# Performance work log

Hardware: AMD Instinct MI355X
Metric: run time of the kernel (lower is better)

## Reference

```python
import jax, jax.numpy as jnp
import numpy as np

K = 9          # top-k neighbors
GROUPS = 4     # GroupNorm groups
EPS_GN = 1e-5  # torch GroupNorm default eps


def group_norm(x, gamma, beta):
    # x: [B, C, H, W]; normalize over (C/GROUPS, H, W) per group
    B, C, H, W = x.shape
    xg = x.reshape(B, GROUPS, -1)
    mu = xg.mean(axis=-1, keepdims=True)
    var = xg.var(axis=-1, keepdims=True)
    xn = ((xg - mu) / jnp.sqrt(var + EPS_GN)).reshape(B, C, H, W)
    return xn * gamma[None, :, None, None] + beta[None, :, None, None]


def setup_inputs() -> dict:
    key = jax.random.key(0)
    ks = jax.random.split(key, 6)
    B, C, H, W = 32, 128, 45, 45
    std = 1.0 / np.sqrt(C)
    x = jax.random.normal(ks[0], (B, C, H, W), dtype=jnp.float32)
    w1 = jax.random.uniform(ks[1], (C, C), jnp.float32, -std, std)
    b1 = jax.random.uniform(ks[2], (C,), jnp.float32, -std, std)
    w2 = jax.random.uniform(ks[3], (C, C), jnp.float32, -std, std)
    b2 = jax.random.uniform(ks[4], (C,), jnp.float32, -std, std)
    gamma1 = jnp.ones((C,), jnp.float32)
    beta1 = jnp.zeros((C,), jnp.float32)
    gamma2 = jnp.ones((C,), jnp.float32)
    beta2 = jnp.zeros((C,), jnp.float32)
    return {"x": x, "w1": w1, "b1": b1, "w2": w2, "b2": b2,
            "gamma1": gamma1, "beta1": beta1, "gamma2": gamma2, "beta2": beta2}


def reference(x, w1, b1, w2, b2, gamma1, beta1, gamma2, beta2):
    B, C, H, W = x.shape
    N = H * W
    # build_knn: flatten, L2-normalize, cosine sim, top-k
    xf = x.reshape(B, C, N).transpose(0, 2, 1)                  # [B, N, C]
    nrm = jnp.linalg.norm(xf, axis=-1, keepdims=True)
    xn = xf / jnp.maximum(nrm, 1e-12)                           # F.normalize
    sim = jnp.einsum('bnc,bmc->bnm', xn, xn)                    # [B, N, N]
    val, idx = jax.lax.top_k(sim, K)                            # [B, N, K]
    # normalized edge weights (shared by both GCN layers)
    v = val / (val.sum(axis=-1, keepdims=True) + 1e-6)          # [B, N, K]

    def gcn_apply(feat, w, b):
        xt = feat @ w                                           # [B, N, C]
        neigh = jax.vmap(lambda t, i: t[i])(xt, idx)            # [B, N, K, C]
        return jnp.einsum('bnkc,bnk->bnc', neigh, v) + b

    out = gcn_apply(xn, w1, b1)
    out = jax.nn.silu(group_norm(out.transpose(0, 2, 1).reshape(B, C, H, W), gamma1, beta1))
    of = out.reshape(B, C, N).transpose(0, 2, 1)
    out = gcn_apply(of, w2, b2)
    out = jax.nn.silu(group_norm(out.transpose(0, 2, 1).reshape(B, C, H, W), gamma2, beta2))
    return out
```

## Files before the change

kernel.cpp:

```cpp
#include <hip/hip_runtime.h>
#include <hip/hip_bf16.h>

#define BN 32
#define CC 128
#define NN 2025
#define KK 9
#define NGROUP 4
#define CPG 32
#define GN_EPS 1e-5f
#define ROWS_TOTAL (BN * NN)

typedef _Float16 f16;
typedef __attribute__((ext_vector_type(8))) _Float16 f16x8;
typedef __attribute__((ext_vector_type(4))) float f32x4;

#define S28 3.725290298461914e-09f
#define S40 9.094947017729282e-13f
#define RH  6.103515625e-05f
#define RL  1.4901161193847656e-08f

#define T0F 0.17f
#define CAP 128

__global__ __launch_bounds__(256) void k_normalize(const float* __restrict__ x,
                                                   f16* __restrict__ xh, f16* __restrict__ xl) {
    int wid  = blockIdx.x * 4 + (threadIdx.x >> 6);
    int lane = threadIdx.x & 63;
    int b = wid / NN;
    int n = wid - b * NN;
    float v0 = x[(b * CC + lane) * NN + n];
    float v1 = x[(b * CC + lane + 64) * NN + n];
    float ss = v0 * v0 + v1 * v1;
#pragma unroll
    for (int off = 32; off > 0; off >>= 1) ss += __shfl_xor(ss, off);
    float s = 1.0f / fmaxf(sqrtf(ss), 1e-12f);
    v0 *= s; v1 *= s;
    float w0 = v0 * 16384.0f, w1 = v1 * 16384.0f;
    f16 h0 = (f16)w0, h1 = (f16)w1;
    f16 l0 = (f16)((w0 - (float)h0) * 4096.0f);
    f16 l1 = (f16)((w1 - (float)h1) * 4096.0f);
    size_t base = (size_t)wid * CC;
    xh[base + lane] = h0;  xh[base + lane + 64] = h1;
    xl[base + lane] = l0;  xl[base + lane + 64] = l1;
}

__device__ __forceinline__ void ins9(float cand, int m, float* v, int* ix,
                                     float& mv, int& mi, int& mp) {
    bool take = (cand > mv) || ((cand == mv) && (m < mi));
    if (take) {
#pragma unroll
        for (int k = 0; k < 9; ++k) if (k == mp) { v[k] = cand; ix[k] = m; }
        float nv = v[0]; int ni = ix[0]; int np = 0;
#pragma unroll
        for (int k = 1; k < 9; ++k) {
            if (v[k] < nv || (v[k] == nv && ix[k] > ni)) { nv = v[k]; ni = ix[k]; np = k; }
        }
        mv = nv; mi = ni; mp = np;
    }
}

__global__ __launch_bounds__(256) void k_sim_topk(const f16* __restrict__ xh, const f16* __restrict__ xl,
                                                  float* __restrict__ vout, int* __restrict__ iout) {
    __shared__ float sv[32][CAP];
    __shared__ int   si[32][CAP];
    __shared__ int   cnt[32];
    __shared__ int   nbad;
    __shared__ int   badrows[32];

    const int b    = blockIdx.y;
    const int r0   = blockIdx.x * 32;
    const int t    = threadIdx.x;
    const int w    = t >> 6;
    const int lane = t & 63;
    const int jr   = lane & 15;
    const int q    = lane >> 4;

    if (t < 32) cnt[t] = 0;
    if (t == 0) nbad = 0;

    f16x8 bh[2][4], bl[2][4];
#pragma unroll
    for (int tile = 0; tile < 2; ++tile) {
        int rr = b * NN + min(r0 + tile * 16 + jr, NN - 1);
        const f16* pH = xh + (size_t)rr * CC;
        const f16* pL = xl + (size_t)rr * CC;
#pragma unroll
        for (int s = 0; s < 4; ++s) {
            bh[tile][s] = *(const f16x8*)(pH + s * 32 + q * 8);
            bl[tile][s] = *(const f16x8*)(pL + s * 32 + q * 8);
        }
    }
    __syncthreads();

    for (int chunk = 0; chunk < 32; ++chunk) {
        const int mb = chunk * 64 + w * 16;
        const int marow = b * NN + min(mb + jr, NN - 1);
        const f16* aHp = xh + (size_t)marow * CC;
        const f16* aLp = xl + (size_t)marow * CC;
        f32x4 h0 = {0.f, 0.f, 0.f, 0.f}, l0 = {0.f, 0.f, 0.f, 0.f};
        f32x4 h1 = {0.f, 0.f, 0.f, 0.f}, l1 = {0.f, 0.f, 0.f, 0.f};
#pragma unroll
        for (int s = 0; s < 4; ++s) {
            f16x8 ah = *(const f16x8*)(aHp + s * 32 + q * 8);
            f16x8 al = *(const f16x8*)(aLp + s * 32 + q * 8);
            h0 = __builtin_amdgcn_mfma_f32_16x16x32_f16(ah, bh[0][s], h0, 0, 0, 0);
            l0 = __builtin_amdgcn_mfma_f32_16x16x32_f16(ah, bl[0][s], l0, 0, 0, 0);
            l0 = __builtin_amdgcn_mfma_f32_16x16x32_f16(al, bh[0][s], l0, 0, 0, 0);
            h1 = __builtin_amdgcn_mfma_f32_16x16x32_f16(ah, bh[1][s], h1, 0, 0, 0);
            l1 = __builtin_amdgcn_mfma_f32_16x16x32_f16(ah, bl[1][s], l1, 0, 0, 0);
            l1 = __builtin_amdgcn_mfma_f32_16x16x32_f16(al, bh[1][s], l1, 0, 0, 0);
        }
#pragma unroll
        for (int reg = 0; reg < 4; ++reg) {
            int m = mb + q * 4 + reg;
            float c0 = h0[reg] * S28 + l0[reg] * S40;
            if (m < NN && c0 > T0F) {
                int pos = atomicAdd(&cnt[jr], 1);
                if (pos < CAP) { sv[jr][pos] = c0; si[jr][pos] = m; }
            }
            float c1 = h1[reg] * S28 + l1[reg] * S40;
            if (m < NN && c1 > T0F) {
                int pos = atomicAdd(&cnt[16 + jr], 1);
                if (pos < CAP) { sv[16 + jr][pos] = c1; si[16 + jr][pos] = m; }
            }
        }
    }
    __syncthreads();

    if (t < 32) {
        int r = r0 + t;
        if (r < NN) {
            int c = cnt[t];
            if (c >= 9 && c <= CAP) {
                float fv[9]; int fi[9];
#pragma unroll
                for (int k = 0; k < 9; ++k) { fv[k] = -3.0e38f; fi[k] = 0x7fffffff; }
                float mv = -3.0e38f; int mi = 0x7fffffff; int mp = 0;
                for (int j = 0; j < c; ++j) ins9(sv[t][j], si[t][j], fv, fi, mv, mi, mp);
                float s = 1e-6f;
#pragma unroll
                for (int k = 0; k < 9; ++k) s += fv[k];
                float inv = 1.0f / s;
                int base = (b * NN + r) * KK;
#pragma unroll
                for (int k = 0; k < 9; ++k) { vout[base + k] = fv[k] * inv; iout[base + k] = fi[k]; }
            } else {
                int slot = atomicAdd(&nbad, 1);
                badrows[slot] = r;
            }
        }
    }
    __syncthreads();

    if (w == 0) {
        int nb = nbad;
        for (int ib = 0; ib < nb; ++ib) {
            int r = badrows[ib];
            const f16* rH = xh + ((size_t)b * NN + r) * CC;
            const f16* rL = xl + ((size_t)b * NN + r) * CC;
            float fv[9]; int fi[9];
#pragma unroll
            for (int k = 0; k < 9; ++k) { fv[k] = -3.0e38f; fi[k] = 0x7fffffff; }
            float mv = -3.0e38f; int mi = 0x7fffffff; int mp = 0;
            for (int m = lane; m < NN; m += 64) {
                const f16* mH = xh + ((size_t)b * NN + m) * CC;
                const f16* mL = xl + ((size_t)b * NN + m) * CC;
                float a1 = 0.f, a2 = 0.f;
                for (int c2 = 0; c2 < CC; ++c2) {
                    float hr = (float)rH[c2], hm = (float)mH[c2];
                    float lr = (float)rL[c2], lm = (float)mL[c2];
                    a1 += hr * hm;
                    a2 += hr * lm + lr * hm;
                }
                ins9(a1 * S28 + a2 * S40, m, fv, fi, mv, mi, mp);
            }
#pragma unroll
            for (int off = 1; off < 64; off <<= 1) {
                float pv[9]; int pi[9];
#pragma unroll
                for (int k = 0; k < 9; ++k) { pv[k] = __shfl_xor(fv[k], off); pi[k] = __shfl_xor(fi[k], off); }
#pragma unroll
                for (int k = 0; k < 9; ++k) ins9(pv[k], pi[k], fv, fi, mv, mi, mp);
            }
            if (lane == 0) {
                float s = 1e-6f;
#pragma unroll
                for (int k = 0; k < 9; ++k) s += fv[k];
                float inv = 1.0f / s;
                int base = (b * NN + r) * KK;
#pragma unroll
                for (int k = 0; k < 9; ++k) { vout[base + k] = fv[k] * inv; iout[base + k] = fi[k]; }
            }
        }
    }
}

#define RST 36
__global__ __launch_bounds__(256) void k_gemm_hl(const f16* __restrict__ xh, const f16* __restrict__ xl,
                                                 const float* __restrict__ w, float* __restrict__ out) {
    __shared__ float rowsT[CC * RST];
    int t = threadIdx.x;
    int row0 = blockIdx.x * 32;
    for (int it = 0; it < 16; ++it) {
        int qq = t + it * 256;
        int c = qq & 127, r = qq >> 7;
        size_t idx = (size_t)(row0 + r) * CC + c;
        rowsT[c * RST + r] = (float)xh[idx] * RH + (float)xl[idx] * RL;
    }
    __syncthreads();
    int j = t & 127, half = t >> 7;
    float acc[16];
#pragma unroll
    for (int r = 0; r < 16; ++r) acc[r] = 0.0f;
    for (int c = 0; c < CC; ++c) {
        float wv = w[c * CC + j];
        const float4* ap = (const float4*)&rowsT[c * RST + half * 16];
        float4 a0 = ap[0], a1 = ap[1], a2 = ap[2], a3 = ap[3];
        acc[0]  += a0.x * wv; acc[1]  += a0.y * wv; acc[2]  += a0.z * wv; acc[3]  += a0.w * wv;
        acc[4]  += a1.x * wv; acc[5]  += a1.y * wv; acc[6]  += a1.z * wv; acc[7]  += a1.w * wv;
        acc[8]  += a2.x * wv; acc[9]  += a2.y * wv; acc[10] += a2.z * wv; acc[11] += a2.w * wv;
        acc[12] += a3.x * wv; acc[13] += a3.y * wv; acc[14] += a3.z * wv; acc[15] += a3.w * wv;
    }
#pragma unroll
    for (int r = 0; r < 16; ++r) out[(size_t)(row0 + half * 16 + r) * CC + j] = acc[r];
}

__global__ __launch_bounds__(256) void k_gemm(const float* __restrict__ in,
                                              const float* __restrict__ w,
                                              float* __restrict__ out) {
    __shared__ float rowsT[CC * RST];
    int t = threadIdx.x;
    int row0 = blockIdx.x * 32;
    for (int it = 0; it < 16; ++it) {
        int qq = t + it * 256;
        int c = qq & 127, r = qq >> 7;
        rowsT[c * RST + r] = in[(size_t)(row0 + r) * CC + c];
    }
    __syncthreads();
    int j = t & 127, half = t >> 7;
    float acc[16];
#pragma unroll
    for (int r = 0; r < 16; ++r) acc[r] = 0.0f;
    for (int c = 0; c < CC; ++c) {
        float wv = w[c * CC + j];
        const float4* ap = (const float4*)&rowsT[c * RST + half * 16];
        float4 a0 = ap[0], a1 = ap[1], a2 = ap[2], a3 = ap[3];
        acc[0]  += a0.x * wv; acc[1]  += a0.y * wv; acc[2]  += a0.z * wv; acc[3]  += a0.w * wv;
        acc[4]  += a1.x * wv; acc[5]  += a1.y * wv; acc[6]  += a1.z * wv; acc[7]  += a1.w * wv;
        acc[8]  += a2.x * wv; acc[9]  += a2.y * wv; acc[10] += a2.z * wv; acc[11] += a2.w * wv;
        acc[12] += a3.x * wv; acc[13] += a3.y * wv; acc[14] += a3.z * wv; acc[15] += a3.w * wv;
    }
#pragma unroll
    for (int r = 0; r < 16; ++r) out[(size_t)(row0 + half * 16 + r) * CC + j] = acc[r];
}

__global__ __launch_bounds__(256) void k_gather(const float* __restrict__ xt,
                                                const float* __restrict__ v,
                                                const int* __restrict__ idx,
                                                const float* __restrict__ bias,
                                                float* __restrict__ out) {
    int t = threadIdx.x;
    int g = blockIdx.x * 2 + (t >> 7);
    int c = t & 127;
    if (g >= ROWS_TOTAL) return;
    int b = g / NN;
    int nb = b * NN;
    float acc = bias[c];
    int base = g * KK;
#pragma unroll
    for (int k = 0; k < KK; ++k) {
        int   ii = idx[base + k];
        float vv = v[base + k];
        acc += vv * xt[(size_t)(nb + ii) * CC + c];
    }
    out[(size_t)g * CC + c] = acc;
}

__global__ __launch_bounds__(256) void k_gnstats(const float* __restrict__ xin,
                                                 float* __restrict__ stats) {
    int bg = blockIdx.x; int b = bg >> 2; int gg = bg & 3;
    size_t base = (size_t)b * (NN * CC) + gg * CPG;
    float s1 = 0.f, s2 = 0.f;
    for (int i = threadIdx.x; i < NN * CPG; i += 256) {
        float x = xin[base + (size_t)(i >> 5) * CC + (i & 31)];
        s1 += x; s2 += x * x;
    }
#pragma unroll
    for (int off = 32; off > 0; off >>= 1) { s1 += __shfl_xor(s1, off); s2 += __shfl_xor(s2, off); }
    __shared__ float r1[4], r2[4];
    int w = threadIdx.x >> 6;
    if ((threadIdx.x & 63) == 0) { r1[w] = s1; r2[w] = s2; }
    __syncthreads();
    if (threadIdx.x == 0) {
        float a = r1[0] + r1[1] + r1[2] + r1[3];
        float qq = r2[0] + r2[1] + r2[2] + r2[3];
        const float inv = 1.0f / (float)(NN * CPG);
        float mean = a * inv;
        float var = qq * inv - mean * mean;
        stats[bg * 2]     = mean;
        stats[bg * 2 + 1] = rsqrtf(fmaxf(var, 0.f) + GN_EPS);
    }
}

__global__ __launch_bounds__(256) void k_gnsilu(const float* __restrict__ xin,
                                                const float* __restrict__ stats,
                                                const float* __restrict__ gamma,
                                                const float* __restrict__ beta,
                                                float* __restrict__ out) {
    size_t e4 = ((size_t)blockIdx.x * 256 + threadIdx.x) * 4;
    int c0 = (int)(e4 & 127);
    int b  = (int)(e4 / (NN * CC));
    int gg = c0 >> 5;
    float mean = stats[(b * 4 + gg) * 2];
    float rstd = stats[(b * 4 + gg) * 2 + 1];
    float4 x = *(const float4*)&xin[e4];
    float g0 = gamma[c0], g1 = gamma[c0 + 1], g2 = gamma[c0 + 2], g3 = gamma[c0 + 3];
    float p0 = beta[c0],  p1 = beta[c0 + 1],  p2 = beta[c0 + 2],  p3 = beta[c0 + 3];
    float y0 = (x.x - mean) * rstd * g0 + p0;
    float y1 = (x.y - mean) * rstd * g1 + p1;
    float y2 = (x.z - mean) * rstd * g2 + p2;
    float y3 = (x.w - mean) * rstd * g3 + p3;
    float4 r;
    r.x = y0 / (1.0f + expf(-y0));
    r.y = y1 / (1.0f + expf(-y1));
    r.z = y2 / (1.0f + expf(-y2));
    r.w = y3 / (1.0f + expf(-y3));
    *(float4*)&out[e4] = r;
}

__global__ __launch_bounds__(256) void k_gnsilu_out(const float* __restrict__ xin,
                                                    const float* __restrict__ stats,
                                                    const float* __restrict__ gamma,
                                                    const float* __restrict__ beta,
                                                    float* __restrict__ out) {
    __shared__ float tile[32 * 65];
    int b = blockIdx.z, ct = blockIdx.y, nt = blockIdx.x;
    int c0 = ct * 32, n0 = nt * 64;
    int t = threadIdx.x;
    int cj = t & 31, ni0 = t >> 5;
    int gg = c0 >> 5;
    float mean = stats[(b * 4 + gg) * 2];
    float rstd = stats[(b * 4 + gg) * 2 + 1];
    float gm = gamma[c0 + cj];
    float bt = beta[c0 + cj];
#pragma unroll
    for (int i = 0; i < 8; ++i) {
        int n = n0 + ni0 + i * 8;
        if (n < NN) {
            float x = xin[((size_t)b * NN + n) * CC + c0 + cj];
            float y = (x - mean) * rstd * gm + bt;
            y = y / (1.0f + expf(-y));
            tile[cj * 65 + ni0 + i * 8] = y;
        }
    }
    __syncthreads();
    int nj = t & 63, ci0 = t >> 6;
#pragma unroll
    for (int i = 0; i < 8; ++i) {
        int c = ci0 + i * 4;
        int n = n0 + nj;
        if (n < NN) out[((size_t)b * CC + c0 + c) * NN + n] = tile[c * 65 + nj];
    }
}

extern "C" void kernel_launch(void* const* d_in, const int* in_sizes, int n_in,
                              void* d_out, int out_size, void* d_ws, size_t ws_size,
                              hipStream_t stream) {
    const float* x      = (const float*)d_in[0];
    const float* w1     = (const float*)d_in[1];
    const float* b1     = (const float*)d_in[2];
    const float* w2     = (const float*)d_in[3];
    const float* b2     = (const float*)d_in[4];
    const float* gamma1 = (const float*)d_in[5];
    const float* beta1  = (const float*)d_in[6];
    const float* gamma2 = (const float*)d_in[7];
    const float* beta2  = (const float*)d_in[8];
    float* out = (float*)d_out;

    const size_t BIG = (size_t)ROWS_TOTAL * CC;
    float* ws   = (float*)d_ws;
    float* bufB = ws;
    f16*   xh   = (f16*)(ws + BIG);
    f16*   xl   = xh + BIG;
    float* bufA = ws + BIG;
    float* vbuf = ws + 2 * BIG;
    int*   ibuf = (int*)(ws + 2 * BIG + (size_t)ROWS_TOTAL * KK);
    float* stats = ws + 2 * BIG + 2 * (size_t)ROWS_TOTAL * KK;

    k_normalize<<<ROWS_TOTAL / 4, 256, 0, stream>>>(x, xh, xl);
    k_sim_topk<<<dim3(64, BN), 256, 0, stream>>>(xh, xl, vbuf, ibuf);

    k_gemm_hl<<<(ROWS_TOTAL + 31) / 32, 256, 0, stream>>>(xh, xl, w1, bufB);
    k_gather<<<ROWS_TOTAL / 2, 256, 0, stream>>>(bufB, vbuf, ibuf, b1, bufA);
    k_gnstats<<<BN * NGROUP, 256, 0, stream>>>(bufA, stats);
    k_gnsilu<<<(int)(BIG / 1024), 256, 0, stream>>>(bufA, stats, gamma1, beta1, bufB);

    k_gemm<<<(ROWS_TOTAL + 31) / 32, 256, 0, stream>>>(bufB, w2, bufA);
    k_gather<<<ROWS_TOTAL / 2, 256, 0, stream>>>(bufA, vbuf, ibuf, b2, bufB);
    k_gnstats<<<BN * NGROUP, 256, 0, stream>>>(bufB, stats);
    k_gnsilu_out<<<dim3((NN + 63) / 64, NGROUP, BN), 256, 0, stream>>>(bufB, stats, gamma2, beta2, out);
}
```

Baseline: 760.3 us.

## Double-buffer A-tile loads in sim/top-k loop and shrink candidate LDS buffers

The similarity loop now prefetches the next 64-row chunk's hi/lo fp16 A fragments into a second register set while the current chunk runs its MFMAs and threshold filtering. This is meant to hide global-load latency behind compute. Candidate indices in shared memory are stored as unsigned short, and both candidate arrays get padded row strides, which cuts LDS footprint and bank conflicts during the per-row scan. The cost is more VGPRs for the second fragment buffer, which may reduce occupancy.

```diff
diff --git a/kernel.cpp b/kernel.cpp
--- a/kernel.cpp
+++ b/kernel.cpp
@@ -59,10 +59,50 @@
     }
 }
 
+
+#define LOADA(CH, AH, AL) do {                                              \
+    int mb_ = (CH) * 64 + w * 16;                                           \
+    size_t ar_ = (size_t)(b * NN + min(mb_ + jr, NN - 1)) * CC;             \
+    const f16* pH_ = xh + ar_;                                              \
+    const f16* pL_ = xl + ar_;                                              \
+    _Pragma("unroll")                                                       \
+    for (int s_ = 0; s_ < 4; ++s_) {                                        \
+        AH[s_] = *(const f16x8*)(pH_ + s_ * 32 + q * 8);                    \
+        AL[s_] = *(const f16x8*)(pL_ + s_ * 32 + q * 8);                    \
+    } } while (0)
+
+#define COMPUTE(CH, AH, AL) do {                                            \
+    f32x4 h0 = {0.f,0.f,0.f,0.f}, l0 = {0.f,0.f,0.f,0.f};                   \
+    f32x4 h1 = {0.f,0.f,0.f,0.f}, l1 = {0.f,0.f,0.f,0.f};                   \
+    _Pragma("unroll")                                                       \
+    for (int s_ = 0; s_ < 4; ++s_) {                                        \
+        h0 = __builtin_amdgcn_mfma_f32_16x16x32_f16(AH[s_], bh[0][s_], h0, 0, 0, 0); \
+        l0 = __builtin_amdgcn_mfma_f32_16x16x32_f16(AH[s_], bl[0][s_], l0, 0, 0, 0); \
+        l0 = __builtin_amdgcn_mfma_f32_16x16x32_f16(AL[s_], bh[0][s_], l0, 0, 0, 0); \
+        h1 = __builtin_amdgcn_mfma_f32_16x16x32_f16(AH[s_], bh[1][s_], h1, 0, 0, 0); \
+        l1 = __builtin_amdgcn_mfma_f32_16x16x32_f16(AH[s_], bl[1][s_], l1, 0, 0, 0); \
+        l1 = __builtin_amdgcn_mfma_f32_16x16x32_f16(AL[s_], bh[1][s_], l1, 0, 0, 0); \
+    }                                                                       \
+    int mb_ = (CH) * 64 + w * 16;                                           \
+    _Pragma("unroll")                                                       \
+    for (int reg_ = 0; reg_ < 4; ++reg_) {                                  \
+        int m_ = mb_ + q * 4 + reg_;                                        \
+        float c0_ = h0[reg_] * S28 + l0[reg_] * S40;                        \
+        if (m_ < NN && c0_ > T0F) {                                         \
+            int pos_ = atomicAdd(&cnt[jr], 1);                              \
+            if (pos_ < CAP) { sv[jr][pos_] = c0_; si[jr][pos_] = (unsigned short)m_; } \
+        }                                                                   \
+        float c1_ = h1[reg_] * S28 + l1[reg_] * S40;                        \
+        if (m_ < NN && c1_ > T0F) {                                         \
+            int pos_ = atomicAdd(&cnt[16 + jr], 1);                         \
+            if (pos_ < CAP) { sv[16 + jr][pos_] = c1_; si[16 + jr][pos_] = (unsigned short)m_; } \
+        }                                                                   \
+    } } while (0)
+
 __global__ __launch_bounds__(256) void k_sim_topk(const f16* __restrict__ xh, const f16* __restrict__ xl,
                                                   float* __restrict__ vout, int* __restrict__ iout) {
-    __shared__ float sv[32][CAP];
-    __shared__ int   si[32][CAP];
+    __shared__ float          sv[32][129];
+    __shared__ unsigned short si[32][130];
     __shared__ int   cnt[32];
     __shared__ int   nbad;
     __shared__ int   badrows[32];
@@ -92,38 +132,14 @@
     }
     __syncthreads();
 
-    for (int chunk = 0; chunk < 32; ++chunk) {
-        const int mb = chunk * 64 + w * 16;
-        const int marow = b * NN + min(mb + jr, NN - 1);
-        const f16* aHp = xh + (size_t)marow * CC;
-        const f16* aLp = xl + (size_t)marow * CC;
-        f32x4 h0 = {0.f, 0.f, 0.f, 0.f}, l0 = {0.f, 0.f, 0.f, 0.f};
-        f32x4 h1 = {0.f, 0.f, 0.f, 0.f}, l1 = {0.f, 0.f, 0.f, 0.f};
-#pragma unroll
-        for (int s = 0; s < 4; ++s) {
-            f16x8 ah = *(const f16x8*)(aHp + s * 32 + q * 8);
-            f16x8 al = *(const f16x8*)(aLp + s * 32 + q * 8);
-            h0 = __builtin_amdgcn_mfma_f32_16x16x32_f16(ah, bh[0][s], h0, 0, 0, 0);
-            l0 = __builtin_amdgcn_mfma_f32_16x16x32_f16(ah, bl[0][s], l0, 0, 0, 0);
-            l0 = __builtin_amdgcn_mfma_f32_16x16x32_f16(al, bh[0][s], l0, 0, 0, 0);
-            h1 = __builtin_amdgcn_mfma_f32_16x16x32_f16(ah, bh[1][s], h1, 0, 0, 0);
-            l1 = __builtin_amdgcn_mfma_f32_16x16x32_f16(ah, bl[1][s], l1, 0, 0, 0);
-            l1 = __builtin_amdgcn_mfma_f32_16x16x32_f16(al, bh[1][s], l1, 0, 0, 0);
-        }
-#pragma unroll
-        for (int reg = 0; reg < 4; ++reg) {
-            int m = mb + q * 4 + reg;
-            float c0 = h0[reg] * S28 + l0[reg] * S40;
-            if (m < NN && c0 > T0F) {
-                int pos = atomicAdd(&cnt[jr], 1);
-                if (pos < CAP) { sv[jr][pos] = c0; si[jr][pos] = m; }
-            }
-            float c1 = h1[reg] * S28 + l1[reg] * S40;
-            if (m < NN && c1 > T0F) {
-                int pos = atomicAdd(&cnt[16 + jr], 1);
-                if (pos < CAP) { sv[16 + jr][pos] = c1; si[16 + jr][pos] = m; }
-            }
-        }
+    f16x8 aEh[4], aEl[4], aOh[4], aOl[4];
+    LOADA(0, aEh, aEl);
+    for (int it = 0; it < 16; ++it) {
+        const int c0 = it * 2;
+        LOADA(c0 + 1, aOh, aOl);
+        COMPUTE(c0, aEh, aEl);
+        if (it < 15) LOADA(c0 + 2, aEh, aEl);
+        COMPUTE(c0 + 1, aOh, aOl);
     }
     __syncthreads();
 
@@ -136,7 +152,7 @@
 #pragma unroll
                 for (int k = 0; k < 9; ++k) { fv[k] = -3.0e38f; fi[k] = 0x7fffffff; }
                 float mv = -3.0e38f; int mi = 0x7fffffff; int mp = 0;
-                for (int j = 0; j < c; ++j) ins9(sv[t][j], si[t][j], fv, fi, mv, mi, mp);
+                for (int j = 0; j < c; ++j) ins9(sv[t][j], (int)si[t][j], fv, fi, mv, mi, mp);
                 float s = 1e-6f;
 #pragma unroll
                 for (int k = 0; k < 9; ++k) s += fv[k];
```

Result: faster. 720.7 us (-5.2%).
